# Performance work log

Measured on AMD Instinct MI355X. Metric: run time of the kernel, lower is better.

Reference implementation:

```python
import jax, jax.numpy as jnp
import numpy as np


def setup_inputs() -> dict:
    key = jax.random.key(0)
    qkv = jax.random.normal(key, (2, 1536, 4096), dtype=jnp.float32)
    return {"qkv": qkv, "num_heads": 8}


def reference(qkv, num_heads):
    bs, width, length = qkv.shape
    ch = width // (3 * num_heads)
    # [B*H, 3*ch, T] -> split into q, k, v each [B*H, ch, T]
    qkv_h = qkv.reshape(bs * num_heads, 3 * ch, length)
    q, k, v = qkv_h[:, :ch], qkv_h[:, ch:2 * ch], qkv_h[:, 2 * ch:]
    scale = 1.0 / np.sqrt(np.sqrt(ch)).astype(np.float32)
    # scores: [B*H, T, T]
    weight = jnp.einsum('bct,bcs->bts', q * scale, k * scale)
    weight = jax.nn.softmax(weight.astype(jnp.float32), axis=-1).astype(weight.dtype)
    a = jnp.einsum('bts,bcs->bct', weight, v)  # [B*H, ch, T]
    return a.reshape(bs, num_heads * ch, length)
```

## Files before the change

### kernel.cpp

```cpp
#include <hip/hip_runtime.h>
#include <hip/hip_bf16.h>

typedef __bf16 bf16x8 __attribute__((ext_vector_type(8)));
typedef __bf16 bf16x4 __attribute__((ext_vector_type(4)));
typedef __bf16 bf16x2 __attribute__((ext_vector_type(2)));
typedef float  f32x4  __attribute__((ext_vector_type(4)));

#define T_LEN 4096
#define QBLK  128
#define KVBLK 64
#define NKV   (T_LEN / KVBLK)

__device__ __forceinline__ int swz(int row, int colByte) {
    return row * 128 + (colByte ^ (((row ^ (row >> 2)) & 7) << 4));
}
__device__ __forceinline__ int swzM(int row, int colByte) {
    return row * 128 + (colByte ^ ((row & 7) << 4));
}
__device__ __forceinline__ int swzO(int row, int colByte) {
    return row * 512 + (colByte ^ ((row & 7) << 5));
}

#define QSCALE 0.18033688011112042f

#if __has_builtin(__builtin_amdgcn_exp2f)
#define EXP2(x) __builtin_amdgcn_exp2f(x)
#else
__device__ __forceinline__ float EXP2(float x) {
    float r; asm("v_exp_f32 %0, %1" : "=v"(r) : "v"(x)); return r;
}
#endif

__global__ __launch_bounds__(512, 4)
void qkv_attn_kernel(const float* __restrict__ qkv, float* __restrict__ out) {
    __shared__ __align__(16) char lds[66560];

    const int fid   = (blockIdx.x & 7) * 64 + (blockIdx.x >> 3);
    const int bh    = fid >> 5;
    const int ttile = fid & 31;
    const float* qp = qkv + (size_t)bh * 192 * T_LEN;
    const float* kp = qp + (size_t)64  * T_LEN;
    const float* vp = qp + (size_t)128 * T_LEN;
    const int t0 = ttile * QBLK;

    const int tid  = threadIdx.x;
    const int wave = tid >> 6, lane = tid & 63;
    const int g = lane >> 4, i = lane & 15;
    const int tg = wave >> 1, half = wave & 1;

    const int k_c  = tid >> 4;
    const int k_sq = (tid & 15) * 4;
    const float* kbase = kp + (size_t)(k_c * 2) * T_LEN + k_sq;
    const int v_c  = tid >> 3;
    const int v_u0 = (tid & 7) * 2;
    const float* vbase = vp + (size_t)v_c * T_LEN + v_u0 * 4;

    {
        const int tq  = (tid & 31) * 4;
        const int cp8 = tid >> 5;
        #pragma unroll
        for (int hh = 0; hh < 2; ++hh) {
            const int cpair = cp8 + hh * 16;
            const float* base = qp + (size_t)(cpair * 2) * T_LEN + t0 + tq;
            float4 lo = *(const float4*)(base);
            float4 hi = *(const float4*)(base + T_LEN);
            bf16x2 v;
            v[0] = (__bf16)(lo.x * QSCALE); v[1] = (__bf16)(hi.x * QSCALE);
            *(bf16x2*)(lds + swz(tq + 0, cpair * 4)) = v;
            v[0] = (__bf16)(lo.y * QSCALE); v[1] = (__bf16)(hi.y * QSCALE);
            *(bf16x2*)(lds + swz(tq + 1, cpair * 4)) = v;
            v[0] = (__bf16)(lo.z * QSCALE); v[1] = (__bf16)(hi.z * QSCALE);
            *(bf16x2*)(lds + swz(tq + 2, cpair * 4)) = v;
            v[0] = (__bf16)(lo.w * QSCALE); v[1] = (__bf16)(hi.w * QSCALE);
            *(bf16x2*)(lds + swz(tq + 3, cpair * 4)) = v;
        }
    }
    {
        float4 lo = *(const float4*)(kbase);
        float4 hi = *(const float4*)(kbase + T_LEN);
        bf16x2 w;
        char* KsW = lds + 16384;
        w[0] = (__bf16)lo.x; w[1] = (__bf16)hi.x; *(bf16x2*)(KsW + swz(k_sq + 0, k_c * 4)) = w;
        w[0] = (__bf16)lo.y; w[1] = (__bf16)hi.y; *(bf16x2*)(KsW + swz(k_sq + 1, k_c * 4)) = w;
        w[0] = (__bf16)lo.z; w[1] = (__bf16)hi.z; *(bf16x2*)(KsW + swz(k_sq + 2, k_c * 4)) = w;
        w[0] = (__bf16)lo.w; w[1] = (__bf16)hi.w; *(bf16x2*)(KsW + swz(k_sq + 3, k_c * 4)) = w;
        char* VsW = lds + 32768;
        #pragma unroll
        for (int p = 0; p < 2; ++p) {
            int u  = v_u0 + p;
            int up = (u & 8) | ((u & 3) << 1) | ((u >> 2) & 1);
            float4 f = *(const float4*)(vbase + p * 4);
            bf16x4 hv;
            hv[0] = (__bf16)f.x; hv[1] = (__bf16)f.y;
            hv[2] = (__bf16)f.z; hv[3] = (__bf16)f.w;
            *(bf16x4*)(VsW + swz(v_c, up * 8)) = hv;
        }
    }
    __syncthreads();
    bf16x8 qreg[2][2];
    #pragma unroll
    for (int h = 0; h < 2; ++h)
        #pragma unroll
        for (int kk = 0; kk < 2; ++kk)
            qreg[h][kk] = *(const bf16x8*)(lds + swz(tg * 32 + h * 16 + i, kk * 64 + g * 16));

    f32x4 oacc[2][4];
    #pragma unroll
    for (int h = 0; h < 2; ++h)
        #pragma unroll
        for (int n = 0; n < 4; ++n) oacc[h][n] = (f32x4){0.f, 0.f, 0.f, 0.f};
    float l0 = 0.f, l1 = 0.f;

    for (int kv = 0; kv < NKV; ++kv) {
        const int s0n = (kv + 1 < NKV) ? (kv + 1) * KVBLK : 0;
        float4 klo = *(const float4*)(kbase + s0n);
        float4 khi = *(const float4*)(kbase + T_LEN + s0n);
        float4 vl0 = *(const float4*)(vbase + s0n);
        float4 vl1 = *(const float4*)(vbase + s0n + 4);

        char* KsR = lds + 16384 + (kv & 1) * 8192;
        char* VsR = lds + 32768 + (kv & 1) * 8192;
        f32x4 sacc[2][2];
        #pragma unroll
        for (int h = 0; h < 2; ++h)
            #pragma unroll
            for (int mt = 0; mt < 2; ++mt) sacc[h][mt] = (f32x4){0.f, 0.f, 0.f, 0.f};
        #pragma unroll
        for (int kk = 0; kk < 2; ++kk)
            #pragma unroll
            for (int mt = 0; mt < 2; ++mt) {
                bf16x8 kf = *(const bf16x8*)(KsR + swz(half * 32 + mt * 16 + i, kk * 64 + g * 16));
                sacc[0][mt] = __builtin_amdgcn_mfma_f32_16x16x32_bf16(kf, qreg[0][kk], sacc[0][mt], 0, 0, 0);
                sacc[1][mt] = __builtin_amdgcn_mfma_f32_16x16x32_bf16(kf, qreg[1][kk], sacc[1][mt], 0, 0, 0);
            }
        float rs0 = 0.f, rs1 = 0.f;
        bf16x8 pa0, pa1;
        #pragma unroll
        for (int r = 0; r < 4; ++r) {
            float a0 = EXP2(sacc[0][0][r]);
            float a1 = EXP2(sacc[0][1][r]);
            rs0 += a0 + a1;
            pa0[r] = (__bf16)a0; pa0[4 + r] = (__bf16)a1;
            float b0 = EXP2(sacc[1][0][r]);
            float b1 = EXP2(sacc[1][1][r]);
            rs1 += b0 + b1;
            pa1[r] = (__bf16)b0; pa1[4 + r] = (__bf16)b1;
        }
        #pragma unroll
        for (int n = 0; n < 4; ++n) {
            bf16x8 bv = *(const bf16x8*)(VsR + swz(n * 16 + i, half * 64 + g * 16));
            oacc[0][n] = __builtin_amdgcn_mfma_f32_16x16x32_bf16(pa0, bv, oacc[0][n], 0, 0, 0);
            oacc[1][n] = __builtin_amdgcn_mfma_f32_16x16x32_bf16(pa1, bv, oacc[1][n], 0, 0, 0);
        }
        rs0 += __shfl_xor(rs0, 16); rs0 += __shfl_xor(rs0, 32);
        rs1 += __shfl_xor(rs1, 16); rs1 += __shfl_xor(rs1, 32);
        l0 += rs0; l1 += rs1;

        if (kv + 1 < NKV) {
            char* KsW = lds + 16384 + ((kv + 1) & 1) * 8192;
            char* VsW = lds + 32768 + ((kv + 1) & 1) * 8192;
            bf16x2 w;
            w[0] = (__bf16)klo.x; w[1] = (__bf16)khi.x; *(bf16x2*)(KsW + swz(k_sq + 0, k_c * 4)) = w;
            w[0] = (__bf16)klo.y; w[1] = (__bf16)khi.y; *(bf16x2*)(KsW + swz(k_sq + 1, k_c * 4)) = w;
            w[0] = (__bf16)klo.z; w[1] = (__bf16)khi.z; *(bf16x2*)(KsW + swz(k_sq + 2, k_c * 4)) = w;
            w[0] = (__bf16)klo.w; w[1] = (__bf16)khi.w; *(bf16x2*)(KsW + swz(k_sq + 3, k_c * 4)) = w;
            #pragma unroll
            for (int p = 0; p < 2; ++p) {
                int u  = v_u0 + p;
                int up = (u & 8) | ((u & 3) << 1) | ((u >> 2) & 1);
                float4 f = p ? vl1 : vl0;
                bf16x4 hv;
                hv[0] = (__bf16)f.x; hv[1] = (__bf16)f.y;
                hv[2] = (__bf16)f.z; hv[3] = (__bf16)f.w;
                *(bf16x4*)(VsW + swz(v_c, up * 8)) = hv;
            }
        }
        __syncthreads();
    }

    char* mbase = lds + 32768 + tg * 8192;
    float* lbase = (float*)(lds + 65536);
    if (half == 1) {
        #pragma unroll
        for (int h = 0; h < 2; ++h)
            #pragma unroll
            for (int n = 0; n < 4; ++n)
                *(f32x4*)(mbase + swzM(n * 16 + i, h * 64 + g * 16)) = oacc[h][n];
        if (g == 0) { lbase[tg * 32 + i] = l0; lbase[tg * 32 + 16 + i] = l1; }
    }
    __syncthreads();
    if (half == 0) {
        #pragma unroll
        for (int h = 0; h < 2; ++h)
            #pragma unroll
            for (int n = 0; n < 4; ++n) {
                f32x4 part = *(const f32x4*)(mbase + swzM(n * 16 + i, h * 64 + g * 16));
                oacc[h][n] += part;
            }
        l0 += lbase[tg * 32 + i];
        l1 += lbase[tg * 32 + 16 + i];
        #pragma unroll
        for (int h = 0; h < 2; ++h) {
            float invl = 1.0f / (h ? l1 : l0);
            #pragma unroll
            for (int reg = 0; reg < 4; ++reg) {
                float inv_r = __shfl(invl, g * 4 + reg);
                int t_loc = tg * 32 + h * 16 + g * 4 + reg;
                #pragma unroll
                for (int n = 0; n < 4; ++n) {
                    int c = n * 16 + i;
                    *(float*)(lds + swzO(c, t_loc * 4)) = oacc[h][n][reg] * inv_r;
                }
            }
        }
    }
    __syncthreads();
    #pragma unroll
    for (int it = 0; it < 4; ++it) {
        int idx = it * 512 + tid;
        int c   = idx >> 5;
        int seg = idx & 31;
        float4 u = *(const float4*)(lds + swzO(c, seg * 16));
        *(float4*)(out + (size_t)(bh * 64 + c) * T_LEN + t0 + seg * 4) = u;
    }
}

extern "C" void kernel_launch(void* const* d_in, const int* in_sizes, int n_in,
                              void* d_out, int out_size, void* d_ws, size_t ws_size,
                              hipStream_t stream) {
    const float* qkv = (const float*)d_in[0];
    float* out = (float*)d_out;
    qkv_attn_kernel<<<dim3(512), dim3(512), 0, stream>>>(qkv, out);
}
```

Before: 107.3 us.

## Pre-convert K/V to swizzled bf16 panels and stream them via global_load_lds

Adds a prepass kernel that converts K and V from fp32 into bf16 tiles already in the swizzled LDS layout and writes them to workspace. The attention kernel then copies each tile straight into LDS with global_load_lds. This removes the per-iteration register staging and conversion work and halves the K/V bytes each block reads. In exchange it adds an extra launch, a workspace round-trip and a dependence on workspace size, and keeps the old kernel as a fallback.

```diff
diff --git a/kernel.cpp b/kernel.cpp
--- a/kernel.cpp
+++ b/kernel.cpp
@@ -31,16 +31,58 @@
 }
 #endif
 
+__device__ __forceinline__ void glds16(const void* g, void* l) {
+    __builtin_amdgcn_global_load_lds(
+        (const __attribute__((address_space(1))) void*)g,
+        (__attribute__((address_space(3))) void*)l, 16, 0, 0);
+}
+
+__global__ __launch_bounds__(256)
+void qkv_prepass(const float* __restrict__ qkv, char* __restrict__ kpan,
+                 char* __restrict__ vpan) {
+    const int tile = blockIdx.x;
+    const int bh   = blockIdx.y;
+    const float* kp = qkv + ((size_t)bh * 192 + 64)  * T_LEN + tile * 64;
+    const float* vp = qkv + ((size_t)bh * 192 + 128) * T_LEN + tile * 64;
+    char* kout = kpan + (size_t)(bh * 64 + tile) * 8192;
+    char* vout = vpan + (size_t)(bh * 64 + tile) * 8192;
+
+    const int t  = threadIdx.x;
+    const int s  = t & 63;
+    const int o4 = t >> 6;
+    #pragma unroll
+    for (int oo = 0; oo < 2; ++oo) {
+        const int oct = o4 + oo * 4;
+        bf16x8 v;
+        #pragma unroll
+        for (int j = 0; j < 8; ++j)
+            v[j] = (__bf16)kp[(size_t)(oct * 8 + j) * T_LEN + s];
+        *(bf16x8*)(kout + swz(s, oct * 16)) = v;
+    }
+    const int c = t & 63;
+    #pragma unroll
+    for (int p = 0; p < 4; ++p) {
+        const int u = o4 * 4 + p;
+        float4 f = *(const float4*)(vp + (size_t)c * T_LEN + u * 4);
+        const int up = (u & 8) | ((u & 3) << 1) | ((u >> 2) & 1);
+        bf16x4 hv;
+        hv[0] = (__bf16)f.x; hv[1] = (__bf16)f.y;
+        hv[2] = (__bf16)f.z; hv[3] = (__bf16)f.w;
+        *(bf16x4*)(vout + swz(c, up * 8)) = hv;
+    }
+}
+
 __global__ __launch_bounds__(512, 4)
-void qkv_attn_kernel(const float* __restrict__ qkv, float* __restrict__ out) {
-    __shared__ __align__(16) char lds[66560];
+void qkv_attn_glds(const float* __restrict__ qkv, float* __restrict__ out,
+                   const char* __restrict__ kpan, const char* __restrict__ vpan) {
+    __shared__ __align__(16) char lds[49664];
 
     const int fid   = (blockIdx.x & 7) * 64 + (blockIdx.x >> 3);
     const int bh    = fid >> 5;
     const int ttile = fid & 31;
     const float* qp = qkv + (size_t)bh * 192 * T_LEN;
-    const float* kp = qp + (size_t)64  * T_LEN;
-    const float* vp = qp + (size_t)128 * T_LEN;
+    const char* kpb = kpan + (size_t)bh * 64 * 8192;
+    const char* vpb = vpan + (size_t)bh * 64 * 8192;
     const int t0 = ttile * QBLK;
 
     const int tid  = threadIdx.x;
@@ -48,12 +90,8 @@
     const int g = lane >> 4, i = lane & 15;
     const int tg = wave >> 1, half = wave & 1;
 
-    const int k_c  = tid >> 4;
-    const int k_sq = (tid & 15) * 4;
-    const float* kbase = kp + (size_t)(k_c * 2) * T_LEN + k_sq;
-    const int v_c  = tid >> 3;
-    const int v_u0 = (tid & 7) * 2;
-    const float* vbase = vp + (size_t)v_c * T_LEN + v_u0 * 4;
+    glds16(kpb + tid * 16, lds + 16384 + wave * 1024);
+    glds16(vpb + tid * 16, lds + 32768 + wave * 1024);
 
     {
         const int tq  = (tid & 31) * 4;
@@ -75,6 +113,157 @@
             *(bf16x2*)(lds + swz(tq + 3, cpair * 4)) = v;
         }
     }
+    __syncthreads();
+    bf16x8 qreg[2][2];
+    #pragma unroll
+    for (int h = 0; h < 2; ++h)
+        #pragma unroll
+        for (int kk = 0; kk < 2; ++kk)
+            qreg[h][kk] = *(const bf16x8*)(lds + swz(tg * 32 + h * 16 + i, kk * 64 + g * 16));
+
+    f32x4 oacc[2][4];
+    #pragma unroll
+    for (int h = 0; h < 2; ++h)
+        #pragma unroll
+        for (int n = 0; n < 4; ++n) oacc[h][n] = (f32x4){0.f, 0.f, 0.f, 0.f};
+    float l0 = 0.f, l1 = 0.f;
+
+    for (int kv = 0; kv < NKV; ++kv) {
+        if (kv + 1 < NKV) {
+            const int b = (kv + 1) & 1;
+            glds16(kpb + (size_t)(kv + 1) * 8192 + tid * 16,
+                   lds + 16384 + b * 8192 + wave * 1024);
+            glds16(vpb + (size_t)(kv + 1) * 8192 + tid * 16,
+                   lds + 32768 + b * 8192 + wave * 1024);
+        }
+        char* KsR = lds + 16384 + (kv & 1) * 8192;
+        char* VsR = lds + 32768 + (kv & 1) * 8192;
+        f32x4 sacc[2][2];
+        #pragma unroll
+        for (int h = 0; h < 2; ++h)
+            #pragma unroll
+            for (int mt = 0; mt < 2; ++mt) sacc[h][mt] = (f32x4){0.f, 0.f, 0.f, 0.f};
+        #pragma unroll
+        for (int kk = 0; kk < 2; ++kk)
+            #pragma unroll
+            for (int mt = 0; mt < 2; ++mt) {
+                bf16x8 kf = *(const bf16x8*)(KsR + swz(half * 32 + mt * 16 + i, kk * 64 + g * 16));
+                sacc[0][mt] = __builtin_amdgcn_mfma_f32_16x16x32_bf16(kf, qreg[0][kk], sacc[0][mt], 0, 0, 0);
+                sacc[1][mt] = __builtin_amdgcn_mfma_f32_16x16x32_bf16(kf, qreg[1][kk], sacc[1][mt], 0, 0, 0);
+            }
+        float rs0 = 0.f, rs1 = 0.f;
+        bf16x8 pa0, pa1;
+        #pragma unroll
+        for (int r = 0; r < 4; ++r) {
+            float a0 = EXP2(sacc[0][0][r]);
+            float a1 = EXP2(sacc[0][1][r]);
+            rs0 += a0 + a1;
+            pa0[r] = (__bf16)a0; pa0[4 + r] = (__bf16)a1;
+            float b0 = EXP2(sacc[1][0][r]);
+            float b1 = EXP2(sacc[1][1][r]);
+            rs1 += b0 + b1;
+            pa1[r] = (__bf16)b0; pa1[4 + r] = (__bf16)b1;
+        }
+        #pragma unroll
+        for (int n = 0; n < 4; ++n) {
+            bf16x8 bv = *(const bf16x8*)(VsR + swz(n * 16 + i, half * 64 + g * 16));
+            oacc[0][n] = __builtin_amdgcn_mfma_f32_16x16x32_bf16(pa0, bv, oacc[0][n], 0, 0, 0);
+            oacc[1][n] = __builtin_amdgcn_mfma_f32_16x16x32_bf16(pa1, bv, oacc[1][n], 0, 0, 0);
+        }
+        rs0 += __shfl_xor(rs0, 16); rs0 += __shfl_xor(rs0, 32);
+        rs1 += __shfl_xor(rs1, 16); rs1 += __shfl_xor(rs1, 32);
+        l0 += rs0; l1 += rs1;
+        __syncthreads();
+    }
+
+    char* mbase = lds + 16384 + tg * 8192;
+    float* lbase = (float*)(lds + 49152);
+    if (half == 1) {
+        #pragma unroll
+        for (int h = 0; h < 2; ++h)
+            #pragma unroll
+            for (int n = 0; n < 4; ++n)
+                *(f32x4*)(mbase + swzM(n * 16 + i, h * 64 + g * 16)) = oacc[h][n];
+        if (g == 0) { lbase[tg * 32 + i] = l0; lbase[tg * 32 + 16 + i] = l1; }
+    }
+    __syncthreads();
+    if (half == 0) {
+        #pragma unroll
+        for (int h = 0; h < 2; ++h)
+            #pragma unroll
+            for (int n = 0; n < 4; ++n)
+                oacc[h][n] += *(const f32x4*)(mbase + swzM(n * 16 + i, h * 64 + g * 16));
+        l0 += lbase[tg * 32 + i];
+        l1 += lbase[tg * 32 + 16 + i];
+    }
+    __syncthreads();
+    if (half == 0) {
+        #pragma unroll
+        for (int h = 0; h < 2; ++h) {
+            float invl = 1.0f / (h ? l1 : l0);
+            #pragma unroll
+            for (int reg = 0; reg < 4; ++reg) {
+                float inv_r = __shfl(invl, g * 4 + reg);
+                int t_loc = tg * 32 + h * 16 + g * 4 + reg;
+                #pragma unroll
+                for (int n = 0; n < 4; ++n) {
+                    int c = n * 16 + i;
+                    *(float*)(lds + swzO(c, t_loc * 4)) = oacc[h][n][reg] * inv_r;
+                }
+            }
+        }
+    }
+    __syncthreads();
+    #pragma unroll
+    for (int it = 0; it < 4; ++it) {
+        int idx = it * 512 + tid;
+        int c   = idx >> 5;
+        int seg = idx & 31;
+        float4 u = *(const float4*)(lds + swzO(c, seg * 16));
+        *(float4*)(out + (size_t)(bh * 64 + c) * T_LEN + t0 + seg * 4) = u;
+    }
+}
+
+__global__ __launch_bounds__(512, 4)
+void qkv_attn_fb(const float* __restrict__ qkv, float* __restrict__ out) {
+    __shared__ __align__(16) char lds[66560];
+    const int fid   = (blockIdx.x & 7) * 64 + (blockIdx.x >> 3);
+    const int bh    = fid >> 5;
+    const int ttile = fid & 31;
+    const float* qp = qkv + (size_t)bh * 192 * T_LEN;
+    const float* kp = qp + (size_t)64  * T_LEN;
+    const float* vp = qp + (size_t)128 * T_LEN;
+    const int t0 = ttile * QBLK;
+    const int tid  = threadIdx.x;
+    const int wave = tid >> 6, lane = tid & 63;
+    const int g = lane >> 4, i = lane & 15;
+    const int tg = wave >> 1, half = wave & 1;
+    const int k_c  = tid >> 4;
+    const int k_sq = (tid & 15) * 4;
+    const float* kbase = kp + (size_t)(k_c * 2) * T_LEN + k_sq;
+    const int v_c  = tid >> 3;
+    const int v_u0 = (tid & 7) * 2;
+    const float* vbase = vp + (size_t)v_c * T_LEN + v_u0 * 4;
+    {
+        const int tq  = (tid & 31) * 4;
+        const int cp8 = tid >> 5;
+        #pragma unroll
+        for (int hh = 0; hh < 2; ++hh) {
+            const int cpair = cp8 + hh * 16;
+            const float* base = qp + (size_t)(cpair * 2) * T_LEN + t0 + tq;
+            float4 lo = *(const float4*)(base);
+            float4 hi = *(const float4*)(base + T_LEN);
+            bf16x2 v;
+            v[0] = (__bf16)(lo.x * QSCALE); v[1] = (__bf16)(hi.x * QSCALE);
+            *(bf16x2*)(lds + swz(tq + 0, cpair * 4)) = v;
+            v[0] = (__bf16)(lo.y * QSCALE); v[1] = (__bf16)(hi.y * QSCALE);
+            *(bf16x2*)(lds + swz(tq + 1, cpair * 4)) = v;
+            v[0] = (__bf16)(lo.z * QSCALE); v[1] = (__bf16)(hi.z * QSCALE);
+            *(bf16x2*)(lds + swz(tq + 2, cpair * 4)) = v;
+            v[0] = (__bf16)(lo.w * QSCALE); v[1] = (__bf16)(hi.w * QSCALE);
+            *(bf16x2*)(lds + swz(tq + 3, cpair * 4)) = v;
+        }
+    }
     {
         float4 lo = *(const float4*)(kbase);
         float4 hi = *(const float4*)(kbase + T_LEN);
@@ -103,21 +292,18 @@
         #pragma unroll
         for (int kk = 0; kk < 2; ++kk)
             qreg[h][kk] = *(const bf16x8*)(lds + swz(tg * 32 + h * 16 + i, kk * 64 + g * 16));
-
     f32x4 oacc[2][4];
     #pragma unroll
     for (int h = 0; h < 2; ++h)
         #pragma unroll
         for (int n = 0; n < 4; ++n) oacc[h][n] = (f32x4){0.f, 0.f, 0.f, 0.f};
     float l0 = 0.f, l1 = 0.f;
-
     for (int kv = 0; kv < NKV; ++kv) {
         const int s0n = (kv + 1 < NKV) ? (kv + 1) * KVBLK : 0;
         float4 klo = *(const float4*)(kbase + s0n);
         float4 khi = *(const float4*)(kbase + T_LEN + s0n);
         float4 vl0 = *(const float4*)(vbase + s0n);
         float4 vl1 = *(const float4*)(vbase + s0n + 4);
-
         char* KsR = lds + 16384 + (kv & 1) * 8192;
         char* VsR = lds + 32768 + (kv & 1) * 8192;
         f32x4 sacc[2][2];
@@ -155,7 +341,6 @@
         rs0 += __shfl_xor(rs0, 16); rs0 += __shfl_xor(rs0, 32);
         rs1 += __shfl_xor(rs1, 16); rs1 += __shfl_xor(rs1, 32);
         l0 += rs0; l1 += rs1;
-
         if (kv + 1 < NKV) {
             char* KsW = lds + 16384 + ((kv + 1) & 1) * 8192;
             char* VsW = lds + 32768 + ((kv + 1) & 1) * 8192;
@@ -177,7 +362,6 @@
         }
         __syncthreads();
     }
-
     char* mbase = lds + 32768 + tg * 8192;
     float* lbase = (float*)(lds + 65536);
     if (half == 1) {
@@ -193,10 +377,8 @@
         #pragma unroll
         for (int h = 0; h < 2; ++h)
             #pragma unroll
-            for (int n = 0; n < 4; ++n) {
-                f32x4 part = *(const f32x4*)(mbase + swzM(n * 16 + i, h * 64 + g * 16));
-                oacc[h][n] += part;
-            }
+            for (int n = 0; n < 4; ++n)
+                oacc[h][n] += *(const f32x4*)(mbase + swzM(n * 16 + i, h * 64 + g * 16));
         l0 += lbase[tg * 32 + i];
         l1 += lbase[tg * 32 + 16 + i];
         #pragma unroll
@@ -230,5 +412,13 @@
                               hipStream_t stream) {
     const float* qkv = (const float*)d_in[0];
     float* out = (float*)d_out;
-    qkv_attn_kernel<<<dim3(512), dim3(512), 0, stream>>>(qkv, out);
-}
+    const size_t pan_bytes = (size_t)16 * 64 * 8192;
+    if (ws_size >= 2 * pan_bytes) {
+        char* kpan = (char*)d_ws;
+        char* vpan = kpan + pan_bytes;
+        qkv_prepass<<<dim3(64, 16), 256, 0, stream>>>(qkv, kpan, vpan);
+        qkv_attn_glds<<<dim3(512), 512, 0, stream>>>(qkv, out, kpan, vpan);
+    } else {
+        qkv_attn_fb<<<dim3(512), 512, 0, stream>>>(qkv, out);
+    }
+}
```

Result: faster. 96.57 us (-10.0%).
